# Kernel optimization log

Measured on AMD Instinct MI355X. Metric: run time of the kernel, lower is better.

Reference implementation:

```python
import jax, jax.numpy as jnp
import numpy as np

N = 100000      # nodes
E = 1200000     # edges
D_IN = 128      # input_dim
H = 64          # hidden_dim
OUT = 3         # output_dim
EPS = 1e-5      # BatchNorm eps


def setup_inputs() -> dict:
    key = jax.random.key(0)
    ks = jax.random.split(key, 24)
    w = lambda k, shape: jax.random.normal(k, shape, jnp.float32) * 0.05
    return {
        "x": jax.random.normal(ks[0], (N, D_IN), jnp.float32),
        "edge_index": jax.random.randint(ks[1], (2, E), 0, N, dtype=jnp.int32),
        "proj_W": w(ks[2], (H, D_IN)), "proj_b": w(ks[3], (H,)),
        "conv1_W": w(ks[4], (H, H)), "conv1_b": w(ks[5], (H,)),
        "bn1_g": jnp.ones((H,), jnp.float32), "bn1_b": w(ks[6], (H,)),
        "conv2_W": w(ks[7], (H, H)), "conv2_b": w(ks[8], (H,)),
        "bn2_g": jnp.ones((H,), jnp.float32), "bn2_b": w(ks[9], (H,)),
        "conv3_W": w(ks[10], (H, H)), "conv3_b": w(ks[11], (H,)),
        "bn3_g": jnp.ones((H,), jnp.float32), "bn3_b": w(ks[12], (H,)),
        "byp_W": w(ks[13], (OUT, D_IN)), "byp_b": w(ks[14], (OUT,)),
        "head_W": w(ks[15], (OUT, H + OUT)), "head_b": w(ks[16], (OUT,)),
    }


def reference(x, edge_index, proj_W, proj_b,
              conv1_W, conv1_b, bn1_g, bn1_b,
              conv2_W, conv2_b, bn2_g, bn2_b,
              conv3_W, conv3_b, bn3_g, bn3_b,
              byp_W, byp_b, head_W, head_b):
    n = x.shape[0]
    row, col = edge_index[0], edge_index[1]
    loop = jnp.arange(n, dtype=row.dtype)
    row_f = jnp.concatenate([row, loop])   # source (with self loops)
    col_f = jnp.concatenate([col, loop])   # target
    # symmetric GCN normalization: deg over targets of A+I, edge weight 1
    deg = jax.ops.segment_sum(jnp.ones(row_f.shape, jnp.float32), col_f, num_segments=n)
    dinv = jnp.where(deg > 0, jax.lax.rsqrt(deg), 0.0)
    norm = dinv[row_f] * dinv[col_f]       # [E+N]

    def gcn(h, W, b):
        h = h @ W.T                                    # transform then propagate
        msg = h[row_f] * norm[:, None]                 # gather + scale
        return jax.ops.segment_sum(msg, col_f, num_segments=n) + b

    def bn(h, g, b):
        # eval-mode BatchNorm1d: running_mean=0, running_var=1 buffers
        return h * (g / jnp.sqrt(1.0 + EPS)) + b

    h = x @ proj_W.T + proj_b
    idn = h
    h = jax.nn.relu(bn(gcn(h, conv1_W, conv1_b), bn1_g, bn1_b)) + idn  # dropout inactive (eval)
    idn = h
    h = jax.nn.relu(bn(gcn(h, conv2_W, conv2_b), bn2_g, bn2_b)) + idn
    h = jax.nn.relu(bn(gcn(h, conv3_W, conv3_b), bn3_g, bn3_b))

    byp = x @ byp_W.T + byp_b
    p = jnp.concatenate([h, byp], axis=1) @ head_W.T + head_b
    kappa = jnp.clip(p[:, 0] * 5.0 + 2.5, 0.2, 10.0)
    alpha = p[:, 1]
    tau = jnp.clip(p[:, 2] + 0.5, 0.05, 2.0)
    return jnp.stack([kappa, alpha, tau], axis=1)
```

## Files before the change

### kernel.cpp

```cpp
#include <hip/hip_runtime.h>
#include <hip/hip_fp16.h>

#define NN 100000
#define NE 1200000
#define NBUK ((NN + 127) / 128)
#define NCHUNK 512
#define NPROJ ((NN + 63) / 64)

typedef _Float16 h8 __attribute__((ext_vector_type(8)));
typedef float f32x4 __attribute__((ext_vector_type(4)));
typedef float f32x2 __attribute__((ext_vector_type(2)));

__global__ __launch_bounds__(256) void k_fusedA(const int* __restrict__ col,
                                                int* __restrict__ blkcnt,
                                                const float* __restrict__ X,
                                                const float* __restrict__ projW,
                                                const float* __restrict__ projb,
                                                const float* __restrict__ bypW,
                                                const float* __restrict__ bypb,
                                                _Float16* __restrict__ Yh,
                                                float* __restrict__ bypOut) {
    constexpr int D = 128, RS = D + 8, KS = D / 32;
    __shared__ _Float16 Xh[64 * RS];
    __shared__ _Float16 Wh[64 * RS];
    const int tid = threadIdx.x;

    if (blockIdx.x < NCHUNK) {
        int* lh = (int*)Xh;
        const int per = (NE + NCHUNK - 1) / NCHUNK;
        const int e0 = blockIdx.x * per;
        const int e1 = (e0 + per < NE) ? (e0 + per) : NE;
        for (int i = tid; i < NBUK; i += 256) lh[i] = 0;
        __syncthreads();
        for (int e = e0 + tid; e < e1; e += 256)
            atomicAdd(&lh[col[e] >> 7], 1);
        __syncthreads();
        for (int b = tid; b < NBUK; b += 256)
            blkcnt[b * NCHUNK + blockIdx.x] = lh[b];
        return;
    }

    const int n0 = (blockIdx.x - NCHUNK) * 64;

    for (int i = tid; i < 64 * (D / 8); i += 256) {
        int j = i / (D / 8), d8 = (i % (D / 8)) * 8;
        const float4* wp = (const float4*)&projW[j * D + d8];
        float4 w0 = wp[0], w1 = wp[1];
        h8 h = { (_Float16)w0.x, (_Float16)w0.y, (_Float16)w0.z, (_Float16)w0.w,
                 (_Float16)w1.x, (_Float16)w1.y, (_Float16)w1.z, (_Float16)w1.w };
        *(h8*)&Wh[j * RS + d8] = h;
    }
    for (int i = tid; i < 64 * (D / 8); i += 256) {
        int nl = i / (D / 8), d8 = (i % (D / 8)) * 8;
        int n = n0 + nl; if (n >= NN) n = NN - 1;
        const float4* xp = (const float4*)&X[(size_t)n * D + d8];
        float4 x0 = xp[0], x1 = xp[1];
        h8 h = { (_Float16)x0.x, (_Float16)x0.y, (_Float16)x0.z, (_Float16)x0.w,
                 (_Float16)x1.x, (_Float16)x1.y, (_Float16)x1.z, (_Float16)x1.w };
        *(h8*)&Xh[nl * RS + d8] = h;
    }
    __syncthreads();

    const int wid = tid >> 6, lane = tid & 63;
    const int lm = lane & 15, lq = lane >> 4;
    const int mBase = wid * 16;

    h8 bfrag[4][KS];
    #pragma unroll
    for (int t = 0; t < 4; ++t)
        #pragma unroll
        for (int s = 0; s < KS; ++s)
            bfrag[t][s] = *(const h8*)&Wh[(t * 16 + lm) * RS + s * 32 + lq * 8];

    h8 bfragB[KS];
    #pragma unroll
    for (int s = 0; s < KS; ++s) {
        if (lm < 3) {
            const float4* wp = (const float4*)&bypW[lm * D + s * 32 + lq * 8];
            float4 w0 = wp[0], w1 = wp[1];
            bfragB[s] = (h8){ (_Float16)w0.x, (_Float16)w0.y, (_Float16)w0.z, (_Float16)w0.w,
                              (_Float16)w1.x, (_Float16)w1.y, (_Float16)w1.z, (_Float16)w1.w };
        } else {
            bfragB[s] = (h8)(_Float16)0;
        }
    }

    f32x4 acc[5] = {};
    #pragma unroll
    for (int s = 0; s < KS; ++s) {
        h8 a = *(const h8*)&Xh[(mBase + lm) * RS + s * 32 + lq * 8];
        #pragma unroll
        for (int t = 0; t < 4; ++t)
            acc[t] = __builtin_amdgcn_mfma_f32_16x16x32_f16(a, bfrag[t][s], acc[t], 0, 0, 0);
        acc[4] = __builtin_amdgcn_mfma_f32_16x16x32_f16(a, bfragB[s], acc[4], 0, 0, 0);
    }

    float bb[4];
    #pragma unroll
    for (int t = 0; t < 4; ++t) bb[t] = projb[t * 16 + lm];
    float bypbv = (lm < 3) ? bypb[lm] : 0.f;
    const int nodeBase = n0 + mBase + lq * 4;

    #pragma unroll
    for (int r = 0; r < 4; ++r) {
        int node = nodeBase + r;
        if (node < NN) {
            #pragma unroll
            for (int t = 0; t < 4; ++t)
                Yh[(size_t)node * 64 + t * 16 + lm] = (_Float16)(acc[t][r] + bb[t]);
            if (lm < 3)
                bypOut[node * 3 + lm] = acc[4][r] + bypbv;
        }
    }
}

__global__ __launch_bounds__(1024) void k_scanAll(int* __restrict__ blkcnt,
                                                  int* __restrict__ bcnt) {
    __shared__ int s[1024];
    const int b = blockIdx.x, tid = threadIdx.x;
    int v = (tid < NCHUNK) ? blkcnt[b * NCHUNK + tid] : 0;
    s[tid] = v;
    __syncthreads();
    #pragma unroll
    for (int d = 1; d < 1024; d <<= 1) {
        int t = (tid >= d) ? s[tid - d] : 0;
        __syncthreads();
        s[tid] += t;
        __syncthreads();
    }
    if (tid < NCHUNK) blkcnt[b * NCHUNK + tid] = s[tid] - v;
    if (tid == 1023) bcnt[b] = s[1023];
}

__global__ __launch_bounds__(256) void k_bucketB(const int* __restrict__ row,
                                                 const int* __restrict__ col,
                                                 const int* __restrict__ bcnt,
                                                 const int* __restrict__ blkcnt,
                                                 unsigned* __restrict__ tmp) {
    __shared__ int lh[NBUK];
    __shared__ int part[256];
    const int tid = threadIdx.x;
    int loc[4]; int sum = 0;
    #pragma unroll
    for (int j = 0; j < 4; ++j) {
        int idx = tid * 4 + j;
        loc[j] = sum;
        sum += (idx < NBUK) ? bcnt[idx] : 0;
    }
    part[tid] = sum;
    __syncthreads();
    #pragma unroll
    for (int d = 1; d < 256; d <<= 1) {
        int t = (tid >= d) ? part[tid - d] : 0;
        __syncthreads();
        part[tid] += t;
        __syncthreads();
    }
    const int excl = part[tid] - sum;
    #pragma unroll
    for (int j = 0; j < 4; ++j) {
        int idx = tid * 4 + j;
        if (idx < NBUK)
            lh[idx] = excl + loc[j] + blkcnt[idx * NCHUNK + blockIdx.x];
    }
    __syncthreads();
    const int per = (NE + NCHUNK - 1) / NCHUNK;
    const int e0 = blockIdx.x * per;
    const int e1 = (e0 + per < NE) ? (e0 + per) : NE;
    for (int e = e0 + tid; e < e1; e += 256) {
        int c = col[e], r = row[e];
        int pos = atomicAdd(&lh[c >> 7], 1);
        tmp[pos] = ((unsigned)r << 7) | (unsigned)(c & 127);
    }
}

__global__ __launch_bounds__(256) void k_buildM(const unsigned* __restrict__ tmp,
                                                const int* __restrict__ bcnt,
                                                int* __restrict__ off,
                                                float* __restrict__ dinv,
                                                int* __restrict__ csr_row,
                                                const _Float16* __restrict__ hA,
                                                const float* __restrict__ W1,
                                                unsigned char* __restrict__ Y8) {
    constexpr int RS2 = 72;
    __shared__ int cnt[128], s[128], cur[128];
    __shared__ int red[256];
    __shared__ float dinvL[128];
    __shared__ _Float16 Hs[128 * RS2];
    __shared__ _Float16 WsL[64 * RS2];
    const int b = blockIdx.x, tid = threadIdx.x;

    for (int i = tid; i < 128 * 8; i += 256) {
        int j = i >> 3, d8 = (i & 7) * 8;
        int n = (b << 7) + j; if (n >= NN) n = NN - 1;
        *(h8*)&Hs[j * RS2 + d8] = *(const h8*)&hA[(size_t)n * 64 + d8];
    }
    for (int i = tid; i < 64 * 8; i += 256) {
        int j = i >> 3, d8 = (i & 7) * 8;
        const float4* wp = (const float4*)&W1[j * 64 + d8];
        float4 w0 = wp[0], w1 = wp[1];
        h8 h = { (_Float16)w0.x, (_Float16)w0.y, (_Float16)w0.z, (_Float16)w0.w,
                 (_Float16)w1.x, (_Float16)w1.y, (_Float16)w1.z, (_Float16)w1.w };
        *(h8*)&WsL[j * RS2 + d8] = h;
    }

    int ssum = 0;
    for (int i = tid; i < b; i += 256) ssum += bcnt[i];
    red[tid] = ssum;
    __syncthreads();
    #pragma unroll
    for (int d = 128; d > 0; d >>= 1) {
        if (tid < d) red[tid] += red[tid + d];
        __syncthreads();
    }
    const int seg0 = red[0];
    const int seg1 = seg0 + bcnt[b];
    const int colBase = b << 7;
    const int nCols = (NN - colBase < 128) ? (NN - colBase) : 128;
    if (tid < 128) cnt[tid] = 0;
    __syncthreads();
    for (int i = seg0 + tid; i < seg1; i += 256)
        atomicAdd(&cnt[tmp[i] & 127], 1);
    __syncthreads();
    if (tid < 128) s[tid] = cnt[tid];
    __syncthreads();
    #pragma unroll
    for (int d = 1; d < 128; d <<= 1) {
        int t = (tid < 128 && tid >= d) ? s[tid - d] : 0;
        __syncthreads();
        if (tid < 128) s[tid] += t;
        __syncthreads();
    }
    if (tid < 128) {
        float dv = rsqrtf((float)cnt[tid] + 1.0f);
        dinvL[tid] = dv;
        if (tid < nCols) {
            int exc = seg0 + s[tid] - cnt[tid];
            off[colBase + tid] = exc;
            cur[tid] = exc;
            dinv[colBase + tid] = dv;
        }
    }
    if (b == 0 && tid == 0) off[NN] = NE;
    __syncthreads();
    for (int i = seg0 + tid; i < seg1; i += 256) {
        unsigned v = tmp[i];
        int pos = atomicAdd(&cur[v & 127u], 1);
        csr_row[pos] = (int)(v >> 7);
    }
    __syncthreads();

    const int wid = tid >> 6, lane = tid & 63;
    const int lm = lane & 15, lq = lane >> 4;
    const int mBase = wid * 16;
    h8 cfrag[4][2];
    #pragma unroll
    for (int t = 0; t < 4; ++t)
        #pragma unroll
        for (int sx = 0; sx < 2; ++sx)
            cfrag[t][sx] = *(const h8*)&WsL[(t * 16 + lm) * RS2 + sx * 32 + lq * 8];
    #pragma unroll
    for (int hh = 0; hh < 2; ++hh) {
        const int rb = hh * 64 + mBase;
        f32x4 acc2[4] = {};
        #pragma unroll
        for (int sx = 0; sx < 2; ++sx) {
            h8 a = *(const h8*)&Hs[(rb + lm) * RS2 + sx * 32 + lq * 8];
            #pragma unroll
            for (int t = 0; t < 4; ++t)
                acc2[t] = __builtin_amdgcn_mfma_f32_16x16x32_f16(a, cfrag[t][sx], acc2[t], 0, 0, 0);
        }
        #pragma unroll
        for (int r = 0; r < 4; ++r) {
            int nl = rb + lq * 4 + r;
            int node = colBase + nl;
            if (node < NN) {
                float sdv = dinvL[nl];
                #pragma unroll
                for (int t = 0; t < 4; ++t) {
                    float v = acc2[t][r] * sdv;
                    int pk = __builtin_amdgcn_cvt_pk_fp8_f32(v, v, 0, false);
                    Y8[(size_t)node * 64 + t * 16 + lm] = (unsigned char)(pk & 0xff);
                }
            }
        }
    }
}

template<bool HEAD>
__global__ __launch_bounds__(256) void k_gather(const unsigned char* __restrict__ hB8,
                                                const float* __restrict__ dinv,
                                                const int* __restrict__ off,
                                                const int* __restrict__ csr_row,
                                                const float* __restrict__ convb,
                                                const float* __restrict__ bng,
                                                const float* __restrict__ bnb,
                                                _Float16* __restrict__ hA,
                                                const float* __restrict__ nextW,
                                                unsigned char* __restrict__ Y8,
                                                const float* __restrict__ byp,
                                                const float* __restrict__ headW,
                                                const float* __restrict__ headb,
                                                float* __restrict__ out) {
    constexpr int RS2 = 72;
    __shared__ _Float16 Ws[HEAD ? 1 : 64 * RS2];
    __shared__ _Float16 Hs[HEAD ? 1 : 32 * RS2];
    __shared__ float HWs[HEAD ? 204 : 1];
    const int tid = threadIdx.x;
    if constexpr (HEAD) {
        for (int i = tid; i < 204; i += 256)
            HWs[i] = (i < 201) ? headW[i] : headb[i - 201];
        __syncthreads();
    } else {
        for (int i = tid; i < 64 * 8; i += 256) {
            int j = i >> 3, d8 = (i & 7) * 8;
            const float4* wp = (const float4*)&nextW[j * 64 + d8];
            float4 w0 = wp[0], w1 = wp[1];
            h8 h = { (_Float16)w0.x, (_Float16)w0.y, (_Float16)w0.z, (_Float16)w0.w,
                     (_Float16)w1.x, (_Float16)w1.y, (_Float16)w1.z, (_Float16)w1.w };
            *(h8*)&Ws[j * RS2 + d8] = h;
        }
    }
    const int wid = tid >> 6, lane = tid & 63;
    const int nloc = wid * 8 + (lane >> 3);
    const int n = blockIdx.x * 32 + nloc;
    const int oct = lane & 7;
    const int f0 = oct * 8;

    const int e0 = off[n];
    const int deg = off[n + 1] - e0;
    int m = deg;
    #pragma unroll
    for (int mask = 8; mask < 64; mask <<= 1) {
        int o = __shfl_xor(m, mask, 64);
        m = (o > m) ? o : m;
    }

    const uint2* rows8 = (const uint2*)hB8;
    f32x2 acc[4] = {};
    {
        uint2 selfw = rows8[(size_t)n * 8 + oct];
        acc[0] += __builtin_amdgcn_cvt_pk_f32_fp8(selfw.x, false);
        acc[1] += __builtin_amdgcn_cvt_pk_f32_fp8(selfw.x, true);
        acc[2] += __builtin_amdgcn_cvt_pk_f32_fp8(selfw.y, false);
        acc[3] += __builtin_amdgcn_cvt_pk_f32_fp8(selfw.y, true);
    }
    for (int it = 0; it < m; it += 8) {
        uint2 w[8];
        #pragma unroll
        for (int q = 0; q < 8; ++q) {
            bool vq = it + q < deg;
            int rq = csr_row[vq ? e0 + it + q : 0];
            w[q] = rows8[(size_t)rq * 8 + oct];
            if (!vq) { w[q].x = 0; w[q].y = 0; }
        }
        #pragma unroll
        for (int q = 0; q < 8; ++q) {
            acc[0] += __builtin_amdgcn_cvt_pk_f32_fp8(w[q].x, false);
            acc[1] += __builtin_amdgcn_cvt_pk_f32_fp8(w[q].x, true);
            acc[2] += __builtin_amdgcn_cvt_pk_f32_fp8(w[q].y, false);
            acc[3] += __builtin_amdgcn_cvt_pk_f32_fp8(w[q].y, true);
        }
    }

    const float dv = dinv[n];
    const float bnscale = rsqrtf(1.0f + 1e-5f);
    const float4 cb0 = *(const float4*)&convb[f0], cb1 = *(const float4*)&convb[f0 + 4];
    const float4 g0  = *(const float4*)&bng[f0],  g1  = *(const float4*)&bng[f0 + 4];
    const float4 b0_ = *(const float4*)&bnb[f0],  b1_ = *(const float4*)&bnb[f0 + 4];
    const float cb[8] = { cb0.x, cb0.y, cb0.z, cb0.w, cb1.x, cb1.y, cb1.z, cb1.w };
    const float gg[8] = { g0.x, g0.y, g0.z, g0.w, g1.x, g1.y, g1.z, g1.w };
    const float bb[8] = { b0_.x, b0_.y, b0_.z, b0_.w, b1_.x, b1_.y, b1_.z, b1_.w };
    float v[8];
    #pragma unroll
    for (int j = 0; j < 8; ++j)
        v[j] = fmaxf((acc[j >> 1][j & 1] * dv + cb[j]) * (gg[j] * bnscale) + bb[j], 0.0f);

    if constexpr (!HEAD) {
        size_t o = ((size_t)n << 6) + f0;
        h8 old = *(const h8*)&hA[o];
        #pragma unroll
        for (int j = 0; j < 8; ++j) v[j] += (float)old[j];
        h8 res = { (_Float16)v[0], (_Float16)v[1], (_Float16)v[2], (_Float16)v[3],
                   (_Float16)v[4], (_Float16)v[5], (_Float16)v[6], (_Float16)v[7] };
        *(h8*)&hA[o] = res;
        *(h8*)&Hs[nloc * RS2 + f0] = res;
        __syncthreads();

        const int lm = lane & 15, lq = lane >> 4;
        const int mt = (wid & 1) * 16;
        const int nt = (wid >> 1) * 32;
        h8 afrag[2], bfrag[2][2];
        #pragma unroll
        for (int s = 0; s < 2; ++s)
            afrag[s] = *(const h8*)&Hs[(mt + lm) * RS2 + s * 32 + lq * 8];
        #pragma unroll
        for (int t = 0; t < 2; ++t)
            #pragma unroll
            for (int s = 0; s < 2; ++s)
                bfrag[t][s] = *(const h8*)&Ws[(nt + t * 16 + lm) * RS2 + s * 32 + lq * 8];
        f32x4 acc2[2] = {};
        #pragma unroll
        for (int s = 0; s < 2; ++s)
            #pragma unroll
            for (int t = 0; t < 2; ++t)
                acc2[t] = __builtin_amdgcn_mfma_f32_16x16x32_f16(afrag[s], bfrag[t][s], acc2[t], 0, 0, 0);
        const int nodeBase = blockIdx.x * 32 + mt + lq * 4;
        #pragma unroll
        for (int r = 0; r < 4; ++r) {
            int node = nodeBase + r;
            float sdv = dinv[node];
            #pragma unroll
            for (int t = 0; t < 2; ++t) {
                float vv = acc2[t][r] * sdv;
                int pk = __builtin_amdgcn_cvt_pk_fp8_f32(vv, vv, 0, false);
                Y8[(size_t)node * 64 + nt + t * 16 + lm] = (unsigned char)(pk & 0xff);
            }
        }
    } else {
        float p[3];
        #pragma unroll
        for (int o = 0; o < 3; ++o) {
            float t = 0.f;
            #pragma unroll
            for (int j = 0; j < 8; ++j) t += v[j] * HWs[o * 67 + f0 + j];
            p[o] = t;
        }
        #pragma unroll
        for (int mask = 1; mask < 8; mask <<= 1) {
            #pragma unroll
            for (int o = 0; o < 3; ++o) p[o] += __shfl_xor(p[o], mask, 64);
        }
        if (oct == 0) {
            float by0 = byp[n * 3], by1 = byp[n * 3 + 1], by2 = byp[n * 3 + 2];
            #pragma unroll
            for (int o = 0; o < 3; ++o)
                p[o] += by0 * HWs[o * 67 + 64] + by1 * HWs[o * 67 + 65] + by2 * HWs[o * 67 + 66]
                      + HWs[201 + o];
            float kappa = fminf(fmaxf(p[0] * 5.0f + 2.5f, 0.2f), 10.0f);
            float tau   = fminf(fmaxf(p[2] + 0.5f, 0.05f), 2.0f);
            out[(size_t)n * 3]     = kappa;
            out[(size_t)n * 3 + 1] = p[1];
            out[(size_t)n * 3 + 2] = tau;
        }
    }
}

extern "C" void kernel_launch(void* const* d_in, const int* in_sizes, int n_in,
                              void* d_out, int out_size, void* d_ws, size_t ws_size,
                              hipStream_t stream) {
    const float* x     = (const float*)d_in[0];
    const int*   ei    = (const int*)d_in[1];
    const int*   row   = ei;
    const int*   col   = ei + NE;
    const float* projW = (const float*)d_in[2];
    const float* projb = (const float*)d_in[3];
    const float* convW[3] = { (const float*)d_in[4], (const float*)d_in[8],  (const float*)d_in[12] };
    const float* convb[3] = { (const float*)d_in[5], (const float*)d_in[9],  (const float*)d_in[13] };
    const float* bng[3]   = { (const float*)d_in[6], (const float*)d_in[10], (const float*)d_in[14] };
    const float* bnb[3]   = { (const float*)d_in[7], (const float*)d_in[11], (const float*)d_in[15] };
    const float* bypW  = (const float*)d_in[16];
    const float* bypb  = (const float*)d_in[17];
    const float* headW = (const float*)d_in[18];
    const float* headb = (const float*)d_in[19];
    float* out = (float*)d_out;

    float*    ws   = (float*)d_ws;
    float*    dinv = ws;
    _Float16* hAh  = (_Float16*)(ws + 102400);
    unsigned char* hB8a = (unsigned char*)(hAh + (size_t)NN * 64);
    float*    byp  = (float*)(hB8a + (size_t)NN * 64);
    int*      off     = (int*)(byp + 300032);
    int*      csr_row = off + 100096;
    int*      bcnt    = csr_row + NE;
    int*      blkcnt  = bcnt + 784;
    unsigned char* hB8b = (unsigned char*)(blkcnt + (size_t)NBUK * NCHUNK);
    unsigned* tmp     = (unsigned*)(hB8b + (size_t)NN * 64);

    k_fusedA<<<NCHUNK + NPROJ, 256, 0, stream>>>(
        col, blkcnt, x, projW, projb, bypW, bypb, hAh, byp);
    k_scanAll<<<NBUK, 1024, 0, stream>>>(blkcnt, bcnt);
    k_bucketB<<<NCHUNK, 256, 0, stream>>>(row, col, bcnt, blkcnt, tmp);
    k_buildM<<<NBUK, 256, 0, stream>>>(tmp, bcnt, off, dinv, csr_row,
                                       hAh, convW[0], hB8a);

    k_gather<false><<<NN / 32, 256, 0, stream>>>(
        hB8a, dinv, off, csr_row, convb[0], bng[0], bnb[0], hAh,
        convW[1], hB8b, nullptr, nullptr, nullptr, nullptr);
    k_gather<false><<<NN / 32, 256, 0, stream>>>(
        hB8b, dinv, off, csr_row, convb[1], bng[1], bnb[1], hAh,
        convW[2], hB8a, nullptr, nullptr, nullptr, nullptr);
    k_gather<true><<<NN / 32, 256, 0, stream>>>(
        hB8a, dinv, off, csr_row, convb[2], bng[2], bnb[2], nullptr,
        nullptr, nullptr, byp, headW, headb, out);
}
```

Before: 245.9 us.

## Replace per-chunk bucket scan with global atomic bucket totals and relative cursors

Drops the per-bucket, per-chunk count matrix and its separate scan kernel. Chunks now add their histograms into global bucket totals with atomics, and the scatter kernel recounts its own chunk histogram and claims a slot range inside each bucket through an atomic cursor. This removes one kernel launch and the large blkcnt write and read traffic, at the cost of redundant histogram work and global atomics. Edge order inside a bucket becomes nondeterministic, which can change floating-point summation order if later stages do not sort.

```diff
diff --git a/kernel.cpp b/kernel.cpp
--- a/kernel.cpp
+++ b/kernel.cpp
@@ -12,7 +12,7 @@
 typedef float f32x2 __attribute__((ext_vector_type(2)));
 
 __global__ __launch_bounds__(256) void k_fusedA(const int* __restrict__ col,
-                                                int* __restrict__ blkcnt,
+                                                int* __restrict__ bsum,
                                                 const float* __restrict__ X,
                                                 const float* __restrict__ projW,
                                                 const float* __restrict__ projb,
@@ -35,8 +35,10 @@
         for (int e = e0 + tid; e < e1; e += 256)
             atomicAdd(&lh[col[e] >> 7], 1);
         __syncthreads();
-        for (int b = tid; b < NBUK; b += 256)
-            blkcnt[b * NCHUNK + blockIdx.x] = lh[b];
+        for (int b = tid; b < NBUK; b += 256) {
+            int v = lh[b];
+            if (v) atomicAdd(&bsum[b], v);
+        }
         return;
     }
 
@@ -114,38 +116,31 @@
     }
 }
 
-__global__ __launch_bounds__(1024) void k_scanAll(int* __restrict__ blkcnt,
-                                                  int* __restrict__ bcnt) {
-    __shared__ int s[1024];
-    const int b = blockIdx.x, tid = threadIdx.x;
-    int v = (tid < NCHUNK) ? blkcnt[b * NCHUNK + tid] : 0;
-    s[tid] = v;
-    __syncthreads();
-    #pragma unroll
-    for (int d = 1; d < 1024; d <<= 1) {
-        int t = (tid >= d) ? s[tid - d] : 0;
-        __syncthreads();
-        s[tid] += t;
-        __syncthreads();
-    }
-    if (tid < NCHUNK) blkcnt[b * NCHUNK + tid] = s[tid] - v;
-    if (tid == 1023) bcnt[b] = s[1023];
-}
-
-__global__ __launch_bounds__(256) void k_bucketB(const int* __restrict__ row,
-                                                 const int* __restrict__ col,
-                                                 const int* __restrict__ bcnt,
-                                                 const int* __restrict__ blkcnt,
-                                                 unsigned* __restrict__ tmp) {
+__global__ __launch_bounds__(256) void k_scatterR(const int* __restrict__ row,
+                                                  const int* __restrict__ col,
+                                                  const int* __restrict__ bsum,
+                                                  int* __restrict__ relcur,
+                                                  unsigned* __restrict__ tmp) {
+    __shared__ int cnt[NBUK];
     __shared__ int lh[NBUK];
     __shared__ int part[256];
     const int tid = threadIdx.x;
+    const int per = (NE + NCHUNK - 1) / NCHUNK;
+    const int e0 = blockIdx.x * per;
+    const int e1 = (e0 + per < NE) ? (e0 + per) : NE;
+
+    for (int i = tid; i < NBUK; i += 256) cnt[i] = 0;
+    __syncthreads();
+    for (int e = e0 + tid; e < e1; e += 256)
+        atomicAdd(&cnt[col[e] >> 7], 1);
+    __syncthreads();
+
     int loc[4]; int sum = 0;
     #pragma unroll
     for (int j = 0; j < 4; ++j) {
         int idx = tid * 4 + j;
         loc[j] = sum;
-        sum += (idx < NBUK) ? bcnt[idx] : 0;
+        sum += (idx < NBUK) ? bsum[idx] : 0;
     }
     part[tid] = sum;
     __syncthreads();
@@ -160,13 +155,12 @@
     #pragma unroll
     for (int j = 0; j < 4; ++j) {
         int idx = tid * 4 + j;
-        if (idx < NBUK)
-            lh[idx] = excl + loc[j] + blkcnt[idx * NCHUNK + blockIdx.x];
-    }
-    __syncthreads();
-    const int per = (NE + NCHUNK - 1) / NCHUNK;
-    const int e0 = blockIdx.x * per;
-    const int e1 = (e0 + per < NE) ? (e0 + per) : NE;
+        if (idx < NBUK) {
+            int c = cnt[idx];
+            lh[idx] = (c > 0) ? (excl + loc[j] + atomicAdd(&relcur[idx], c)) : 0;
+        }
+    }
+    __syncthreads();
     for (int e = e0 + tid; e < e1; e += 256) {
         int c = col[e], r = row[e];
         int pos = atomicAdd(&lh[c >> 7], 1);
@@ -472,16 +466,17 @@
     float*    byp  = (float*)(hB8a + (size_t)NN * 64);
     int*      off     = (int*)(byp + 300032);
     int*      csr_row = off + 100096;
-    int*      bcnt    = csr_row + NE;
-    int*      blkcnt  = bcnt + 784;
-    unsigned char* hB8b = (unsigned char*)(blkcnt + (size_t)NBUK * NCHUNK);
+    int*      bsum    = csr_row + NE;
+    int*      relcur  = bsum + 784;
+    unsigned char* hB8b = (unsigned char*)(relcur + 784);
     unsigned* tmp     = (unsigned*)(hB8b + (size_t)NN * 64);
 
+    hipMemsetAsync(bsum, 0, 2 * 784 * sizeof(int), stream);
+
     k_fusedA<<<NCHUNK + NPROJ, 256, 0, stream>>>(
-        col, blkcnt, x, projW, projb, bypW, bypb, hAh, byp);
-    k_scanAll<<<NBUK, 1024, 0, stream>>>(blkcnt, bcnt);
-    k_bucketB<<<NCHUNK, 256, 0, stream>>>(row, col, bcnt, blkcnt, tmp);
-    k_buildM<<<NBUK, 256, 0, stream>>>(tmp, bcnt, off, dinv, csr_row,
+        col, bsum, x, projW, projb, bypW, bypb, hAh, byp);
+    k_scatterR<<<NCHUNK, 256, 0, stream>>>(row, col, bsum, relcur, tmp);
+    k_buildM<<<NBUK, 256, 0, stream>>>(tmp, bsum, off, dinv, csr_row,
                                        hAh, convW[0], hB8a);
 
     k_gather<false><<<NN / 32, 256, 0, stream>>>(
```

After: 283.0 us. 1.15x slower.
